# Performance work log

Measured on AMD Instinct MI355X. Metric: run time of the kernel, lower is better.

## Reference

```python
import jax, jax.numpy as jnp
import numpy as np

N = 100000          # nodes
E = 1000000         # edges (before self loops)
F_IN = 128          # node feature dim
HEADS = [4, 2, 2]   # gat_heads
D = 48              # per-head out channels (hardcoded in module)
G = 64              # number of graphs in batch
FC_DIM = 192
OUT_DIM = 96
NEG_SLOPE = 0.2     # PyG GATConv default


def setup_inputs() -> dict:
    key = jax.random.key(0)
    ks = jax.random.split(key, 32)
    d = {
        "x": jax.random.normal(ks[0], (N, F_IN), jnp.float32),
        "edge_index": jax.random.randint(ks[1], (2, E), 0, N, dtype=jnp.int64),
        "batch": jnp.sort(jax.random.randint(ks[2], (N,), 0, G, dtype=jnp.int64)),
    }
    in_ch = F_IN
    k = 3
    for i, h in enumerate(HEADS):
        d[f"W{i}"] = jax.random.normal(ks[k], (in_ch, h * D), jnp.float32) / np.sqrt(in_ch); k += 1
        d[f"att_src{i}"] = jax.random.normal(ks[k], (h, D), jnp.float32) * 0.1; k += 1
        d[f"att_dst{i}"] = jax.random.normal(ks[k], (h, D), jnp.float32) * 0.1; k += 1
        d[f"bias{i}"] = jnp.zeros((h * D,), jnp.float32)
        in_ch = h * D
    d["fcW1"] = jax.random.normal(ks[k], (in_ch, FC_DIM), jnp.float32) / np.sqrt(in_ch); k += 1
    d["fcb1"] = jnp.zeros((FC_DIM,), jnp.float32)
    d["fcW2"] = jax.random.normal(ks[k], (FC_DIM, OUT_DIM), jnp.float32) / np.sqrt(FC_DIM); k += 1
    d["fcb2"] = jnp.zeros((OUT_DIM,), jnp.float32)
    return d


def _gat_layer(x, W, att_src, att_dst, bias, src, dst, heads):
    n = x.shape[0]
    h = (x @ W).reshape(n, heads, D)                    # [N,H,D]
    a_src = jnp.sum(h * att_src, axis=-1)               # [N,H]
    a_dst = jnp.sum(h * att_dst, axis=-1)               # [N,H]
    e = jax.nn.leaky_relu(a_src[src] + a_dst[dst], NEG_SLOPE)   # [Et,H]
    # segment softmax over incoming edges at each destination node
    m = jax.ops.segment_max(e, dst, num_segments=n)
    e = jnp.exp(e - m[dst])
    denom = jax.ops.segment_sum(e, dst, num_segments=n)
    alpha = e / (denom[dst] + 1e-16)                    # [Et,H]
    msg = h[src] * alpha[..., None]                     # [Et,H,D]
    out = jax.ops.segment_sum(msg, dst, num_segments=n) # [N,H,D]
    return out.reshape(n, heads * D) + bias


def reference(x, edge_index, batch,
              W0, att_src0, att_dst0, bias0,
              W1, att_src1, att_dst1, bias1,
              W2, att_src2, att_dst2, bias2,
              fcW1, fcb1, fcW2, fcb2):
    n = x.shape[0]
    loops = jnp.arange(n, dtype=edge_index.dtype)
    src = jnp.concatenate([edge_index[0], loops])   # add self loops (PyG default)
    dst = jnp.concatenate([edge_index[1], loops])
    x = jax.nn.relu(_gat_layer(x, W0, att_src0, att_dst0, bias0, src, dst, HEADS[0]))
    x = jax.nn.relu(_gat_layer(x, W1, att_src1, att_dst1, bias1, src, dst, HEADS[1]))
    x = jax.nn.relu(_gat_layer(x, W2, att_src2, att_dst2, bias2, src, dst, HEADS[2]))
    # global mean pool over graphs
    sums = jax.ops.segment_sum(x, batch, num_segments=G)
    counts = jax.ops.segment_sum(jnp.ones((n, 1), x.dtype), batch, num_segments=G)
    pooled = sums / jnp.maximum(counts, 1.0)
    h = jax.nn.relu(pooled @ fcW1 + fcb1)
    return h @ fcW2 + fcb2
```

## Files before the change

### kernel.cpp

```cpp
#include <hip/hip_runtime.h>

#define CAP 48
#define DD 48
#define BSH 8
#define NBUCK_MAX 400
#define CHUNK_MAX 4300

typedef short v8s __attribute__((ext_vector_type(8)));
typedef float v4f __attribute__((ext_vector_type(4)));
typedef float v2f __attribute__((ext_vector_type(2)));

__device__ __forceinline__ unsigned int bf16r(float f) {
    unsigned int u = __float_as_uint(f);
    return (u + 0x7FFFu + ((u >> 16) & 1u)) >> 16;
}

__device__ __forceinline__ v8s ld_frag(const ushort* p) {
    const uint2* q = reinterpret_cast<const uint2*>(p);
    uint2 a = q[0], b = q[1];
    union { unsigned int u[4]; v8s v; } t;
    t.u[0] = a.x; t.u[1] = a.y; t.u[2] = b.x; t.u[3] = b.y;
    return t.v;
}


__global__ void hist_kernel(const int* __restrict__ ei, int E, int N, int nbuck,
                            int* __restrict__ Hh) {
    __shared__ int lhist[NBUCK_MAX];
    int blk = blockIdx.x, t = threadIdx.x;
    int Et = E + N;
    int chunk = (Et + 255) >> 8;
    int lo = blk * chunk, hi = min(Et, lo + chunk);
    for (int i = t; i < nbuck; i += 256) lhist[i] = 0;
    __syncthreads();
    for (int e = lo + t; e < hi; e += 256) {
        int d = (e < E) ? ei[E + e] : (e - E);
        atomicAdd(&lhist[d >> BSH], 1);
    }
    __syncthreads();
    for (int b = t; b < nbuck; b += 256) Hh[b * 256 + blk] = lhist[b];
}

__global__ void scan_bucket_kernel(int* __restrict__ Hh, int* __restrict__ btot) {
    int b = blockIdx.x, lane = threadIdx.x;
    uint4 v = reinterpret_cast<uint4*>(Hh)[b * 64 + lane];
    unsigned s0 = v.x, s1 = s0 + v.y, s2 = s1 + v.z, s3 = s2 + v.w;
    unsigned incl = s3;
#pragma unroll
    for (int off = 1; off < 64; off <<= 1) {
        unsigned tmp = __shfl_up(incl, off);
        if (lane >= off) incl += tmp;
    }
    unsigned excl = incl - s3;
    reinterpret_cast<uint4*>(Hh)[b * 64 + lane] =
        make_uint4(excl, excl + s0, excl + s1, excl + s2);
    if (lane == 63) btot[b] = (int)incl;
}

__global__ void scan_base_kernel(const int* __restrict__ btot, int* __restrict__ bbase, int nbuck) {
    int lane = threadIdx.x;
    int carry = 0;
    int nch = (nbuck + 63) >> 6;
    for (int c = 0; c < nch; c++) {
        int idx = c * 64 + lane;
        int val = (idx < nbuck) ? btot[idx] : 0;
        int incl = val;
#pragma unroll
        for (int off = 1; off < 64; off <<= 1) {
            int tmp = __shfl_up(incl, off);
            if (lane >= off) incl += tmp;
        }
        if (idx < nbuck) bbase[idx] = carry + incl - val;
        carry += __shfl(incl, 63);
    }
    if (lane == 0) bbase[nbuck] = carry;
}

__global__ void add_base_kernel(int* __restrict__ Hh, const int* __restrict__ bbase) {
    Hh[blockIdx.x * 256 + threadIdx.x] += bbase[blockIdx.x];
}

__global__ void scatter_kernel(const int* __restrict__ ei, int E, int N, int nbuck,
                               const int* __restrict__ Hh, unsigned int* __restrict__ P) {
    __shared__ unsigned int sp[CHUNK_MAX];
    __shared__ int ga[CHUNK_MAX];
    __shared__ int lhist[NBUCK_MAX], lbaseL[NBUCK_MAX], lbaseG[NBUCK_MAX], lcur[NBUCK_MAX];
    int blk = blockIdx.x, t = threadIdx.x;
    int Et = E + N;
    int chunk = (Et + 255) >> 8;
    int lo = blk * chunk, hi = min(Et, lo + chunk);
    for (int i = t; i < nbuck; i += 256) { lhist[i] = 0; lcur[i] = 0; }
    __syncthreads();
    for (int e = lo + t; e < hi; e += 256) {
        int d = (e < E) ? ei[E + e] : (e - E);
        atomicAdd(&lhist[d >> BSH], 1);
    }
    __syncthreads();
    if (t < 64) {
        int lane = t, carry = 0;
        int nch = (nbuck + 63) >> 6;
        for (int c = 0; c < nch; c++) {
            int idx = c * 64 + lane;
            int val = (idx < nbuck) ? lhist[idx] : 0;
            int incl = val;
#pragma unroll
            for (int off = 1; off < 64; off <<= 1) {
                int tmp = __shfl_up(incl, off);
                if (lane >= off) incl += tmp;
            }
            if (idx < nbuck) {
                lbaseL[idx] = carry + incl - val;
                lbaseG[idx] = Hh[idx * 256 + blk];
            }
            carry += __shfl(incl, 63);
        }
    }
    __syncthreads();
    for (int e = lo + t; e < hi; e += 256) {
        int s, d;
        if (e < E) { s = ei[e]; d = ei[E + e]; } else { s = e - E; d = e - E; }
        int b = d >> BSH;
        int lpos = atomicAdd(&lcur[b], 1);
        int loc = lbaseL[b] + lpos;
        sp[loc] = ((unsigned)(d & 255) << 24) | (unsigned)s;
        ga[loc] = lbaseG[b] + lpos;
    }
    __syncthreads();
    int len = hi - lo;
    for (int i = t; i < len; i += 256) P[ga[i]] = sp[i];
}

__global__ void buildadj_kernel(const unsigned int* __restrict__ P, const int* __restrict__ bbase,
                                int* __restrict__ adj, int* __restrict__ cnt, int N) {
    __shared__ int slab[256 * CAP];
    __shared__ int cntL[256];
    int b = blockIdx.x, t = threadIdx.x;
    int n0 = b << BSH;
    int nodes = min(256, N - n0);
    cntL[t] = 0;
    __syncthreads();
    int lo = bbase[b], hi = bbase[b + 1];
    for (int i = lo + t; i < hi; i += 256) {
        unsigned p = P[i];
        int dloc = (int)(p >> 24);
        int s = (int)(p & 0x1FFFFu);
        int lpos = atomicAdd(&cntL[dloc], 1);
        if (lpos < CAP) slab[dloc * CAP + lpos] = s;
    }
    __syncthreads();
    int tot = nodes * CAP;
    for (int i = t; i < tot; i += 256) adj[(long)n0 * CAP + i] = slab[i];
    if (t < nodes) cnt[n0 + t] = min(cntL[t], CAP);
}

__global__ void cast_x_kernel(const float* __restrict__ x, unsigned int* __restrict__ xb, long n2) {
    long i = (long)blockIdx.x * blockDim.x + threadIdx.x;
    if (i >= n2) return;
    float2 v = reinterpret_cast<const float2*>(x)[i];
    xb[i] = bf16r(v.x) | (bf16r(v.y) << 16);
}

__global__ void convw_kernel(const float* __restrict__ W, ushort* __restrict__ WT, int K, int NC) {
    int i = blockIdx.x * blockDim.x + threadIdx.x;
    if (i >= K * NC) return;
    int k = i / NC, n = i % NC;
    WT[n * K + k] = (ushort)bf16r(W[i]);
}

template<int K, int NCT, int HEADS>
__global__ void gemm_mfma(const ushort* __restrict__ Xb, const ushort* __restrict__ WT,
                          const float* __restrict__ att_s, const float* __restrict__ att_d,
                          ushort* __restrict__ Hb, float* __restrict__ asrc,
                          float* __restrict__ adst, int N) {
    __shared__ ushort XT_l[128 * 40];
    __shared__ ushort WT_l[96 * 40];
    int tid = threadIdx.x;
    int wv = tid >> 6, lane = tid & 63;
    int m = lane & 15, quad = lane >> 4;
    int rb = blockIdx.x * 128;
    int c0 = blockIdx.y * 96;
    int mw = wv * 32;
    v4f acc[2][6];
#pragma unroll
    for (int mi = 0; mi < 2; mi++)
#pragma unroll
        for (int nb = 0; nb < 6; nb++) acc[mi][nb] = (v4f){0.f, 0.f, 0.f, 0.f};

    for (int k0 = 0; k0 < K; k0 += 32) {
#pragma unroll
        for (int t = 0; t < 2; t++) {
            int ch = tid + t * 256;
            int r = ch >> 2, kq = ch & 3;
            int rg = rb + r;
            uint4 v = make_uint4(0u, 0u, 0u, 0u);
            if (rg < N) v = *reinterpret_cast<const uint4*>(&Xb[(long)rg * K + k0 + kq * 8]);
            uint2* d = reinterpret_cast<uint2*>(&XT_l[r * 40 + kq * 8]);
            d[0] = make_uint2(v.x, v.y);
            d[1] = make_uint2(v.z, v.w);
        }
#pragma unroll
        for (int t = 0; t < 2; t++) {
            int ch = tid + t * 256;
            if (ch < 384) {
                int wr = ch >> 2, kq = ch & 3;
                uint4 v = *reinterpret_cast<const uint4*>(&WT[(long)(c0 + wr) * K + k0 + kq * 8]);
                uint2* d = reinterpret_cast<uint2*>(&WT_l[wr * 40 + kq * 8]);
                d[0] = make_uint2(v.x, v.y);
                d[1] = make_uint2(v.z, v.w);
            }
        }
        __syncthreads();
        v8s af[2], bf[6];
        af[0] = ld_frag(&XT_l[(mw + m) * 40 + quad * 8]);
        af[1] = ld_frag(&XT_l[(mw + 16 + m) * 40 + quad * 8]);
#pragma unroll
        for (int nb = 0; nb < 6; nb++)
            bf[nb] = ld_frag(&WT_l[(nb * 16 + m) * 40 + quad * 8]);
#pragma unroll
        for (int mi = 0; mi < 2; mi++)
#pragma unroll
            for (int nb = 0; nb < 6; nb++)
                acc[mi][nb] = __builtin_amdgcn_mfma_f32_16x16x32_bf16(af[mi], bf[nb], acc[mi][nb], 0, 0, 0);
        __syncthreads();
    }

#pragma unroll
    for (int mi = 0; mi < 2; mi++)
#pragma unroll
        for (int r = 0; r < 4; r++) {
            int R = rb + mw + mi * 16 + quad * 4 + r;
            if (R < N) {
#pragma unroll
                for (int nb = 0; nb < 6; nb++)
                    Hb[(long)R * NCT + c0 + nb * 16 + m] = (ushort)bf16r(acc[mi][nb][r]);
            }
        }

    float aS[6], aD[6];
    int h0 = c0 / DD;
#pragma unroll
    for (int nb = 0; nb < 6; nb++) {
        int cb = nb * 16 + m;
        int hl = cb / DD;
        int cih = cb - hl * DD;
        aS[nb] = att_s[(h0 + hl) * DD + cih];
        aD[nb] = att_d[(h0 + hl) * DD + cih];
    }
#pragma unroll
    for (int mi = 0; mi < 2; mi++)
#pragma unroll
        for (int r = 0; r < 4; r++) {
            float ps0 = 0.f, ps1 = 0.f, pd0 = 0.f, pd1 = 0.f;
#pragma unroll
            for (int nb = 0; nb < 3; nb++) {
                ps0 = fmaf(acc[mi][nb][r], aS[nb], ps0);
                pd0 = fmaf(acc[mi][nb][r], aD[nb], pd0);
            }
#pragma unroll
            for (int nb = 3; nb < 6; nb++) {
                ps1 = fmaf(acc[mi][nb][r], aS[nb], ps1);
                pd1 = fmaf(acc[mi][nb][r], aD[nb], pd1);
            }
#pragma unroll
            for (int d = 1; d < 16; d <<= 1) {
                ps0 += __shfl_xor(ps0, d); ps1 += __shfl_xor(ps1, d);
                pd0 += __shfl_xor(pd0, d); pd1 += __shfl_xor(pd1, d);
            }
            int R = rb + mw + mi * 16 + quad * 4 + r;
            if (m == 0 && R < N) {
                asrc[R * HEADS + h0]     = ps0;
                asrc[R * HEADS + h0 + 1] = ps1;
                adst[R * HEADS + h0]     = pd0;
                adst[R * HEADS + h0 + 1] = pd1;
            }
        }
}

template<int OUT, int HEADS, int EPW, bool OBF16>
__global__ void agg_kernel(const unsigned int* __restrict__ Hb,
                           const float* __restrict__ asrc, const float* __restrict__ adst,
                           const int* __restrict__ adj, const int* __restrict__ cnt,
                           const float* __restrict__ bias,
                           unsigned int* __restrict__ Ob, float* __restrict__ Of, int N) {
    constexpr int LPE = 64 / EPW;
    constexpr int ROWU = OUT / 2;
    __shared__ float wlds[4][HEADS][65];
    __shared__ float dlds[4][HEADS];
    __shared__ int   slds[4][64];
    int wv = threadIdx.x >> 6;
    int lane = threadIdx.x & 63;
    int esub = lane / LPE;
    int lp   = lane % LPE;
    int n = blockIdx.x * 4 + wv;
    bool valid = (n < N);
    int nn = valid ? n : 0;
    int deg_raw = cnt[nn];
    int araw = (lane < CAP) ? adj[(long)nn * CAP + lane] : 0;
    int deg = min(deg_raw, CAP);
    int s = (lane < deg) ? araw : 0;
    slds[wv][lane] = s;

    float av[HEADS], dvv[HEADS];
    if constexpr (HEADS == 4) {
        float4 t = *reinterpret_cast<const float4*>(&asrc[s * 4]);
        av[0] = t.x; av[1] = t.y; av[2] = t.z; av[3] = t.w;
        float4 u = *reinterpret_cast<const float4*>(&adst[nn * 4]);
        dvv[0] = u.x; dvv[1] = u.y; dvv[2] = u.z; dvv[3] = u.w;
    } else {
        float2 t = *reinterpret_cast<const float2*>(&asrc[s * 2]);
        av[0] = t.x; av[1] = t.y;
        float2 u = *reinterpret_cast<const float2*>(&adst[nn * 2]);
        dvv[0] = u.x; dvv[1] = u.y;
    }
    float w[HEADS];
#pragma unroll
    for (int h = 0; h < HEADS; h++) {
        float e = av[h] + dvv[h];
        e = (e < 0.f) ? 0.2f * e : e;
        w[h] = (lane < deg) ? __expf(e) : 0.f;
        wlds[wv][h][lane] = w[h];
    }
#pragma unroll
    for (int h = 0; h < HEADS; h++) {
        float dsum = w[h];
#pragma unroll
        for (int off = 1; off < 64; off <<= 1) dsum += __shfl_xor(dsum, off);
        if (lane == 0) dlds[wv][h] = dsum;
    }
    __syncthreads();

    int c = lp * 6;
    int head = c / DD;
    const float* wrow = &wlds[wv][head][0];
    v2f a0 = (v2f){0.f, 0.f}, a1 = (v2f){0.f, 0.f}, a2 = (v2f){0.f, 0.f};

    for (int base = 0; base < deg; base += 2 * EPW) {
        int e0 = base + esub, e1 = base + EPW + esub;
        int s0 = slds[wv][e0], s1 = slds[wv][e1];
        uint3 h0 = *reinterpret_cast<const uint3*>(&Hb[(long)s0 * ROWU + lp * 3]);
        uint3 h1 = *reinterpret_cast<const uint3*>(&Hb[(long)s1 * ROWU + lp * 3]);
        float w0 = wrow[e0], w1 = wrow[e1];
        v2f p;
        p.x = __uint_as_float(h0.x << 16); p.y = __uint_as_float(h0.x & 0xFFFF0000u);
        a0 += w0 * p;
        p.x = __uint_as_float(h0.y << 16); p.y = __uint_as_float(h0.y & 0xFFFF0000u);
        a1 += w0 * p;
        p.x = __uint_as_float(h0.z << 16); p.y = __uint_as_float(h0.z & 0xFFFF0000u);
        a2 += w0 * p;
        p.x = __uint_as_float(h1.x << 16); p.y = __uint_as_float(h1.x & 0xFFFF0000u);
        a0 += w1 * p;
        p.x = __uint_as_float(h1.y << 16); p.y = __uint_as_float(h1.y & 0xFFFF0000u);
        a1 += w1 * p;
        p.x = __uint_as_float(h1.z << 16); p.y = __uint_as_float(h1.z & 0xFFFF0000u);
        a2 += w1 * p;
    }

#pragma unroll
    for (int off = LPE; off < 64; off <<= 1) {
        a0.x += __shfl_xor(a0.x, off); a0.y += __shfl_xor(a0.y, off);
        a1.x += __shfl_xor(a1.x, off); a1.y += __shfl_xor(a1.y, off);
        a2.x += __shfl_xor(a2.x, off); a2.y += __shfl_xor(a2.y, off);
    }

    if (valid && esub == 0) {
        float invd = 1.f / (dlds[wv][head] + 1e-16f);
        float o[6];
        o[0] = fmaxf(fmaf(a0.x, invd, bias[c + 0]), 0.f);
        o[1] = fmaxf(fmaf(a0.y, invd, bias[c + 1]), 0.f);
        o[2] = fmaxf(fmaf(a1.x, invd, bias[c + 2]), 0.f);
        o[3] = fmaxf(fmaf(a1.y, invd, bias[c + 3]), 0.f);
        o[4] = fmaxf(fmaf(a2.x, invd, bias[c + 4]), 0.f);
        o[5] = fmaxf(fmaf(a2.y, invd, bias[c + 5]), 0.f);
        if (OBF16) {
            uint3 pk;
            pk.x = bf16r(o[0]) | (bf16r(o[1]) << 16);
            pk.y = bf16r(o[2]) | (bf16r(o[3]) << 16);
            pk.z = bf16r(o[4]) | (bf16r(o[5]) << 16);
            *reinterpret_cast<uint3*>(&Ob[(long)n * ROWU + lp * 3]) = pk;
        } else {
            float* dst = &Of[(long)n * OUT + c];
            *reinterpret_cast<float2*>(dst)     = make_float2(o[0], o[1]);
            *reinterpret_cast<float2*>(dst + 2) = make_float2(o[2], o[3]);
            *reinterpret_cast<float2*>(dst + 4) = make_float2(o[4], o[5]);
        }
    }
}

__global__ void pool_kernel(const float* __restrict__ O, const int* __restrict__ batch,
                            float* __restrict__ sums, float* __restrict__ counts, int N) {
    int grp = threadIdx.x >> 7;
    int c = threadIdx.x & 127;
    int n0 = (blockIdx.x * 4 + grp) * 64;
    if (n0 >= N) return;
    int nend = min(N, n0 + 64);
    bool act = (c < 96);
    float acc = 0.f; int cl = 0;
    int cur = batch[n0];
    int n = n0;
    for (; n + 4 <= nend; n += 4) {
        int g0 = batch[n], g1 = batch[n + 1], g2 = batch[n + 2], g3 = batch[n + 3];
        float v0 = 0.f, v1 = 0.f, v2 = 0.f, v3 = 0.f;
        if (act) {
            v0 = O[(long)n * 96 + c];       v1 = O[(long)(n + 1) * 96 + c];
            v2 = O[(long)(n + 2) * 96 + c]; v3 = O[(long)(n + 3) * 96 + c];
        }
#define POOL_STEP(g, v)                                                        \
        if ((g) != cur) {                                                      \
            if (act) atomicAdd(&sums[cur * 96 + c], acc);                      \
            if (c == 96) atomicAdd(&counts[cur], (float)cl);                   \
            acc = 0.f; cl = 0; cur = (g);                                      \
        }                                                                      \
        acc += (v); cl++;
        POOL_STEP(g0, v0) POOL_STEP(g1, v1) POOL_STEP(g2, v2) POOL_STEP(g3, v3)
    }
    for (; n < nend; n++) {
        int g = batch[n];
        float v = act ? O[(long)n * 96 + c] : 0.f;
        POOL_STEP(g, v)
    }
#undef POOL_STEP
    if (act) atomicAdd(&sums[cur * 96 + c], acc);
    if (c == 96) atomicAdd(&counts[cur], (float)cl);
}

__global__ void fc_kernel(const float* __restrict__ sums, const float* __restrict__ counts,
                          const float* __restrict__ W1, const float* __restrict__ b1,
                          const float* __restrict__ W2, const float* __restrict__ b2,
                          float* __restrict__ out) {
    __shared__ float p[96];
    __shared__ float h1[192];
    int g = blockIdx.x, tid = threadIdx.x;
    if (tid < 96) p[tid] = sums[g * 96 + tid] / fmaxf(counts[g], 1.0f);
    __syncthreads();
    float s = b1[tid];
    for (int c = 0; c < 96; c++) s = fmaf(p[c], W1[c * 192 + tid], s);
    h1[tid] = fmaxf(s, 0.f);
    __syncthreads();
    if (tid < 96) {
        float s2 = b2[tid];
        for (int j = 0; j < 192; j++) s2 = fmaf(h1[j], W2[j * 96 + tid], s2);
        out[g * 96 + tid] = s2;
    }
}

extern "C" void kernel_launch(void* const* d_in, const int* in_sizes, int n_in,
                              void* d_out, int out_size, void* d_ws, size_t ws_size,
                              hipStream_t stream) {
    const float* x     = (const float*)d_in[0];
    const int*   ei    = (const int*)d_in[1];
    const int*   batch = (const int*)d_in[2];
    const float* W0  = (const float*)d_in[3];
    const float* as0 = (const float*)d_in[4];
    const float* ad0 = (const float*)d_in[5];
    const float* b0  = (const float*)d_in[6];
    const float* W1  = (const float*)d_in[7];
    const float* as1 = (const float*)d_in[8];
    const float* ad1 = (const float*)d_in[9];
    const float* b1  = (const float*)d_in[10];
    const float* W2  = (const float*)d_in[11];
    const float* as2 = (const float*)d_in[12];
    const float* ad2 = (const float*)d_in[13];
    const float* b2  = (const float*)d_in[14];
    const float* fcW1 = (const float*)d_in[15];
    const float* fcb1 = (const float*)d_in[16];
    const float* fcW2 = (const float*)d_in[17];
    const float* fcb2 = (const float*)d_in[18];

    const int N = in_sizes[0] / 128;
    const int E = in_sizes[1] / 2;
    const int Et = E + N;
    const int nbuck = (N + 255) >> 8;

    char* ws = (char*)d_ws;
    unsigned int* Xb   = (unsigned int*)ws;
    unsigned int* Hb   = (unsigned int*)(ws + (size_t)N * 256);
    unsigned int* Ob   = (unsigned int*)(ws + (size_t)N * 640);
    float*        Obuf = (float*)(ws + (size_t)N * 1024);
    float*        ASRC = (float*)(ws + (size_t)N * 1408);
    float*        ADST = (float*)(ws + (size_t)N * 1424);
    int*          ADJ  = (int*)(ws + (size_t)N * 1440);
    int*          CNT  = (int*)(ws + (size_t)N * 1632);
    float*        SUMS = (float*)(ws + (size_t)N * 1636);
    float*        COUNTS = SUMS + 64 * 96;
    ushort*       WT0  = (ushort*)(COUNTS + 64);
    ushort*       WT1  = WT0 + 192 * 128;
    ushort*       WT2  = WT1 + 96 * 192;
    char*         tail = (char*)(WT2 + 96 * 96);
    int*          HIST = (int*)tail;
    int*          BTOT = (int*)(tail + NBUCK_MAX * 256 * 4);
    int*          BBASE = (int*)(tail + NBUCK_MAX * 256 * 4 + NBUCK_MAX * 4);
    unsigned int* P    = (unsigned int*)(tail + NBUCK_MAX * 260 * 4 + 64);

    hipMemsetAsync(SUMS, 0, (64 * 96 + 64) * 4, stream);

    hist_kernel<<<256, 256, 0, stream>>>(ei, E, N, nbuck, HIST);
    scan_bucket_kernel<<<nbuck, 64, 0, stream>>>(HIST, BTOT);
    scan_base_kernel<<<1, 64, 0, stream>>>(BTOT, BBASE, nbuck);
    add_base_kernel<<<nbuck, 256, 0, stream>>>(HIST, BBASE);
    scatter_kernel<<<256, 256, 0, stream>>>(ei, E, N, nbuck, HIST, P);
    buildadj_kernel<<<nbuck, 256, 0, stream>>>(P, BBASE, ADJ, CNT, N);

    long n2 = (long)N * 64;
    cast_x_kernel<<<(int)((n2 + 255) / 256), 256, 0, stream>>>(x, Xb, n2);
    convw_kernel<<<(128 * 192 + 255) / 256, 256, 0, stream>>>(W0, WT0, 128, 192);
    convw_kernel<<<(192 * 96 + 255) / 256, 256, 0, stream>>>(W1, WT1, 192, 96);
    convw_kernel<<<(96 * 96 + 255) / 256, 256, 0, stream>>>(W2, WT2, 96, 96);

    int gb = (N + 127) / 128;

    gemm_mfma<128, 192, 4><<<dim3(gb, 2), 256, 0, stream>>>((const ushort*)Xb, WT0, as0, ad0,
                                                            (ushort*)Hb, ASRC, ADST, N);
    agg_kernel<192, 4, 2, true><<<(N + 3) / 4, 256, 0, stream>>>(Hb, ASRC, ADST, ADJ, CNT, b0, Ob, nullptr, N);

    gemm_mfma<192, 96, 2><<<dim3(gb, 1), 256, 0, stream>>>((const ushort*)Ob, WT1, as1, ad1,
                                                           (ushort*)Hb, ASRC, ADST, N);
    agg_kernel<96, 2, 4, true><<<(N + 3) / 4, 256, 0, stream>>>(Hb, ASRC, ADST, ADJ, CNT, b1, Ob, nullptr, N);

    gemm_mfma<96, 96, 2><<<dim3(gb, 1), 256, 0, stream>>>((const ushort*)Ob, WT2, as2, ad2,
                                                          (ushort*)Hb, ASRC, ADST, N);
    agg_kernel<96, 2, 4, false><<<(N + 3) / 4, 256, 0, stream>>>(Hb, ASRC, ADST, ADJ, CNT, b2, nullptr, Obuf, N);

    pool_kernel<<<(N / 256) + 1, 512, 0, stream>>>(Obuf, batch, SUMS, COUNTS, N);
    fc_kernel<<<64, 192, 0, stream>>>(SUMS, COUNTS, fcW1, fcb1, fcW2, fcb2, (float*)d_out);
}
```

Baseline: 467.4 us.

## Fuse input cast into GEMM, pooling into last aggregation, merge small kernels

```diff
diff --git a/kernel.cpp b/kernel.cpp
--- a/kernel.cpp
+++ b/kernel.cpp
@@ -76,12 +76,9 @@
     if (lane == 0) bbase[nbuck] = carry;
 }
 
-__global__ void add_base_kernel(int* __restrict__ Hh, const int* __restrict__ bbase) {
-    Hh[blockIdx.x * 256 + threadIdx.x] += bbase[blockIdx.x];
-}
-
 __global__ void scatter_kernel(const int* __restrict__ ei, int E, int N, int nbuck,
-                               const int* __restrict__ Hh, unsigned int* __restrict__ P) {
+                               const int* __restrict__ Hh, const int* __restrict__ bbase,
+                               unsigned int* __restrict__ P) {
     __shared__ unsigned int sp[CHUNK_MAX];
     __shared__ int ga[CHUNK_MAX];
     __shared__ int lhist[NBUCK_MAX], lbaseL[NBUCK_MAX], lbaseG[NBUCK_MAX], lcur[NBUCK_MAX];
@@ -110,7 +107,7 @@
             }
             if (idx < nbuck) {
                 lbaseL[idx] = carry + incl - val;
-                lbaseG[idx] = Hh[idx * 256 + blk];
+                lbaseG[idx] = Hh[idx * 256 + blk] + bbase[idx];
             }
             carry += __shfl(incl, 63);
         }
@@ -153,22 +150,24 @@
     if (t < nodes) cnt[n0 + t] = min(cntL[t], CAP);
 }
 
-__global__ void cast_x_kernel(const float* __restrict__ x, unsigned int* __restrict__ xb, long n2) {
-    long i = (long)blockIdx.x * blockDim.x + threadIdx.x;
-    if (i >= n2) return;
-    float2 v = reinterpret_cast<const float2*>(x)[i];
-    xb[i] = bf16r(v.x) | (bf16r(v.y) << 16);
-}
-
-__global__ void convw_kernel(const float* __restrict__ W, ushort* __restrict__ WT, int K, int NC) {
-    int i = blockIdx.x * blockDim.x + threadIdx.x;
-    if (i >= K * NC) return;
-    int k = i / NC, n = i % NC;
-    WT[n * K + k] = (ushort)bf16r(W[i]);
-}
-
-template<int K, int NCT, int HEADS>
-__global__ void gemm_mfma(const ushort* __restrict__ Xb, const ushort* __restrict__ WT,
+__global__ void convw_all_kernel(const float* __restrict__ W0, const float* __restrict__ W1,
+                                 const float* __restrict__ W2, ushort* __restrict__ WT0,
+                                 ushort* __restrict__ WT1, ushort* __restrict__ WT2) {
+    int i = blockIdx.x * 256 + threadIdx.x;
+    if (i < 24576) {
+        int k = i / 192, n = i % 192;
+        WT0[n * 128 + k] = (ushort)bf16r(W0[i]);
+    } else if (i < 43008) {
+        int j = i - 24576; int k = j / 96, n = j % 96;
+        WT1[n * 192 + k] = (ushort)bf16r(W1[j]);
+    } else if (i < 52224) {
+        int j = i - 43008; int k = j / 96, n = j % 96;
+        WT2[n * 96 + k] = (ushort)bf16r(W2[j]);
+    }
+}
+
+template<int K, int NCT, int HEADS, bool XF32>
+__global__ void gemm_mfma(const void* __restrict__ Xp, const ushort* __restrict__ WT,
                           const float* __restrict__ att_s, const float* __restrict__ att_d,
                           ushort* __restrict__ Hb, float* __restrict__ asrc,
                           float* __restrict__ adst, int N) {
@@ -192,11 +191,25 @@
             int ch = tid + t * 256;
             int r = ch >> 2, kq = ch & 3;
             int rg = rb + r;
-            uint4 v = make_uint4(0u, 0u, 0u, 0u);
-            if (rg < N) v = *reinterpret_cast<const uint4*>(&Xb[(long)rg * K + k0 + kq * 8]);
+            uint2 d0, d1;
+            if (XF32) {
+                const float* Xf = (const float*)Xp;
+                float4 va = make_float4(0.f, 0.f, 0.f, 0.f), vb = va;
+                if (rg < N) {
+                    va = *reinterpret_cast<const float4*>(&Xf[(long)rg * K + k0 + kq * 8]);
+                    vb = *reinterpret_cast<const float4*>(&Xf[(long)rg * K + k0 + kq * 8 + 4]);
+                }
+                d0 = make_uint2(bf16r(va.x) | (bf16r(va.y) << 16), bf16r(va.z) | (bf16r(va.w) << 16));
+                d1 = make_uint2(bf16r(vb.x) | (bf16r(vb.y) << 16), bf16r(vb.z) | (bf16r(vb.w) << 16));
+            } else {
+                const ushort* Xb = (const ushort*)Xp;
+                uint4 v = make_uint4(0u, 0u, 0u, 0u);
+                if (rg < N) v = *reinterpret_cast<const uint4*>(&Xb[(long)rg * K + k0 + kq * 8]);
+                d0 = make_uint2(v.x, v.y);
+                d1 = make_uint2(v.z, v.w);
+            }
             uint2* d = reinterpret_cast<uint2*>(&XT_l[r * 40 + kq * 8]);
-            d[0] = make_uint2(v.x, v.y);
-            d[1] = make_uint2(v.z, v.w);
+            d[0] = d0; d[1] = d1;
         }
 #pragma unroll
         for (int t = 0; t < 2; t++) {
@@ -276,17 +289,21 @@
         }
 }
 
-template<int OUT, int HEADS, int EPW, bool OBF16>
+template<int OUT, int HEADS, int EPW, bool OBF16, bool POOL>
 __global__ void agg_kernel(const unsigned int* __restrict__ Hb,
                            const float* __restrict__ asrc, const float* __restrict__ adst,
                            const int* __restrict__ adj, const int* __restrict__ cnt,
                            const float* __restrict__ bias,
-                           unsigned int* __restrict__ Ob, float* __restrict__ Of, int N) {
+                           unsigned int* __restrict__ Ob,
+                           const int* __restrict__ batch,
+                           float* __restrict__ sums, float* __restrict__ counts, int N) {
     constexpr int LPE = 64 / EPW;
     constexpr int ROWU = OUT / 2;
     __shared__ float wlds[4][HEADS][65];
     __shared__ float dlds[4][HEADS];
     __shared__ int   slds[4][64];
+    __shared__ float psum[4][96];
+    __shared__ int   gl[4];
     int wv = threadIdx.x >> 6;
     int lane = threadIdx.x & 63;
     int esub = lane / LPE;
@@ -326,6 +343,9 @@
 #pragma unroll
         for (int off = 1; off < 64; off <<= 1) dsum += __shfl_xor(dsum, off);
         if (lane == 0) dlds[wv][h] = dsum;
+    }
+    if (POOL) {
+        if (lane == 0) gl[wv] = valid ? batch[nn] : -1;
     }
     __syncthreads();
 
@@ -362,65 +382,49 @@
         a2.x += __shfl_xor(a2.x, off); a2.y += __shfl_xor(a2.y, off);
     }
 
-    if (valid && esub == 0) {
-        float invd = 1.f / (dlds[wv][head] + 1e-16f);
-        float o[6];
-        o[0] = fmaxf(fmaf(a0.x, invd, bias[c + 0]), 0.f);
-        o[1] = fmaxf(fmaf(a0.y, invd, bias[c + 1]), 0.f);
-        o[2] = fmaxf(fmaf(a1.x, invd, bias[c + 2]), 0.f);
-        o[3] = fmaxf(fmaf(a1.y, invd, bias[c + 3]), 0.f);
-        o[4] = fmaxf(fmaf(a2.x, invd, bias[c + 4]), 0.f);
-        o[5] = fmaxf(fmaf(a2.y, invd, bias[c + 5]), 0.f);
-        if (OBF16) {
+    float invd = 1.f / (dlds[wv][head] + 1e-16f);
+    float o[6];
+    o[0] = fmaxf(fmaf(a0.x, invd, bias[c + 0]), 0.f);
+    o[1] = fmaxf(fmaf(a0.y, invd, bias[c + 1]), 0.f);
+    o[2] = fmaxf(fmaf(a1.x, invd, bias[c + 2]), 0.f);
+    o[3] = fmaxf(fmaf(a1.y, invd, bias[c + 3]), 0.f);
+    o[4] = fmaxf(fmaf(a2.x, invd, bias[c + 4]), 0.f);
+    o[5] = fmaxf(fmaf(a2.y, invd, bias[c + 5]), 0.f);
+
+    if (POOL) {
+        __syncthreads();
+        bool uni = (gl[0] >= 0) && (gl[1] == gl[0]) && (gl[2] == gl[0]) && (gl[3] == gl[0]);
+        if (uni) {
+            if (esub == 0) {
+#pragma unroll
+                for (int j = 0; j < 6; j++) psum[wv][c + j] = o[j];
+            }
+            __syncthreads();
+            int t = threadIdx.x;
+            if (t < 96) {
+                float sm = psum[0][t] + psum[1][t] + psum[2][t] + psum[3][t];
+                atomicAdd(&sums[gl[0] * 96 + t], sm);
+            } else if (t == 96) {
+                atomicAdd(&counts[gl[0]], 4.0f);
+            }
+        } else {
+            if (valid && esub == 0) {
+                int g = gl[wv];
+#pragma unroll
+                for (int j = 0; j < 6; j++) atomicAdd(&sums[g * 96 + c + j], o[j]);
+                if (lp == 0) atomicAdd(&counts[g], 1.0f);
+            }
+            __syncthreads();
+        }
+    } else {
+        if (valid && esub == 0) {
             uint3 pk;
             pk.x = bf16r(o[0]) | (bf16r(o[1]) << 16);
             pk.y = bf16r(o[2]) | (bf16r(o[3]) << 16);
             pk.z = bf16r(o[4]) | (bf16r(o[5]) << 16);
             *reinterpret_cast<uint3*>(&Ob[(long)n * ROWU + lp * 3]) = pk;
-        } else {
-            float* dst = &Of[(long)n * OUT + c];
-            *reinterpret_cast<float2*>(dst)     = make_float2(o[0], o[1]);
-            *reinterpret_cast<float2*>(dst + 2) = make_float2(o[2], o[3]);
-            *reinterpret_cast<float2*>(dst + 4) = make_float2(o[4], o[5]);
-        }
-    }
-}
-
-__global__ void pool_kernel(const float* __restrict__ O, const int* __restrict__ batch,
-                            float* __restrict__ sums, float* __restrict__ counts, int N) {
-    int grp = threadIdx.x >> 7;
-    int c = threadIdx.x & 127;
-    int n0 = (blockIdx.x * 4 + grp) * 64;
-    if (n0 >= N) return;
-    int nend = min(N, n0 + 64);
-    bool act = (c < 96);
-    float acc = 0.f; int cl = 0;
-    int cur = batch[n0];
-    int n = n0;
-    for (; n + 4 <= nend; n += 4) {
-        int g0 = batch[n], g1 = batch[n + 1], g2 = batch[n + 2], g3 = batch[n + 3];
-        float v0 = 0.f, v1 = 0.f, v2 = 0.f, v3 = 0.f;
-        if (act) {
-            v0 = O[(long)n * 96 + c];       v1 = O[(long)(n + 1) * 96 + c];
-            v2 = O[(long)(n + 2) * 96 + c]; v3 = O[(long)(n + 3) * 96 + c];
-        }
-#define POOL_STEP(g, v)                                                        \
-        if ((g) != cur) {                                                      \
-            if (act) atomicAdd(&sums[cur * 96 + c], acc);                      \
-            if (c == 96) atomicAdd(&counts[cur], (float)cl);                   \
-            acc = 0.f; cl = 0; cur = (g);                                      \
-        }                                                                      \
-        acc += (v); cl++;
-        POOL_STEP(g0, v0) POOL_STEP(g1, v1) POOL_STEP(g2, v2) POOL_STEP(g3, v3)
-    }
-    for (; n < nend; n++) {
-        int g = batch[n];
-        float v = act ? O[(long)n * 96 + c] : 0.f;
-        POOL_STEP(g, v)
-    }
-#undef POOL_STEP
-    if (act) atomicAdd(&sums[cur * 96 + c], acc);
-    if (c == 96) atomicAdd(&counts[cur], (float)cl);
+        }
+    }
 }
 
 __global__ void fc_kernel(const float* __restrict__ sums, const float* __restrict__ counts,
@@ -468,19 +472,16 @@
 
     const int N = in_sizes[0] / 128;
     const int E = in_sizes[1] / 2;
-    const int Et = E + N;
     const int nbuck = (N + 255) >> 8;
 
     char* ws = (char*)d_ws;
-    unsigned int* Xb   = (unsigned int*)ws;
-    unsigned int* Hb   = (unsigned int*)(ws + (size_t)N * 256);
-    unsigned int* Ob   = (unsigned int*)(ws + (size_t)N * 640);
-    float*        Obuf = (float*)(ws + (size_t)N * 1024);
-    float*        ASRC = (float*)(ws + (size_t)N * 1408);
-    float*        ADST = (float*)(ws + (size_t)N * 1424);
-    int*          ADJ  = (int*)(ws + (size_t)N * 1440);
-    int*          CNT  = (int*)(ws + (size_t)N * 1632);
-    float*        SUMS = (float*)(ws + (size_t)N * 1636);
+    unsigned int* Hb   = (unsigned int*)ws;
+    unsigned int* Ob   = (unsigned int*)(ws + (size_t)N * 384);
+    float*        ASRC = (float*)(ws + (size_t)N * 768);
+    float*        ADST = (float*)(ws + (size_t)N * 784);
+    int*          ADJ  = (int*)(ws + (size_t)N * 800);
+    int*          CNT  = (int*)(ws + (size_t)N * 992);
+    float*        SUMS = (float*)(ws + (size_t)N * 996);
     float*        COUNTS = SUMS + 64 * 96;
     ushort*       WT0  = (ushort*)(COUNTS + 64);
     ushort*       WT1  = WT0 + 192 * 128;
@@ -496,30 +497,27 @@
     hist_kernel<<<256, 256, 0, stream>>>(ei, E, N, nbuck, HIST);
     scan_bucket_kernel<<<nbuck, 64, 0, stream>>>(HIST, BTOT);
     scan_base_kernel<<<1, 64, 0, stream>>>(BTOT, BBASE, nbuck);
-    add_base_kernel<<<nbuck, 256, 0, stream>>>(HIST, BBASE);
-    scatter_kernel<<<256, 256, 0, stream>>>(ei, E, N, nbuck, HIST, P);
+    scatter_kernel<<<256, 256, 0, stream>>>(ei, E, N, nbuck, HIST, BBASE, P);
     buildadj_kernel<<<nbuck, 256, 0, stream>>>(P, BBASE, ADJ, CNT, N);
 
-    long n2 = (long)N * 64;
-    cast_x_kernel<<<(int)((n2 + 255) / 256), 256, 0, stream>>>(x, Xb, n2);
-    convw_kernel<<<(128 * 192 + 255) / 256, 256, 0, stream>>>(W0, WT0, 128, 192);
-    convw_kernel<<<(192 * 96 + 255) / 256, 256, 0, stream>>>(W1, WT1, 192, 96);
-    convw_kernel<<<(96 * 96 + 255) / 256, 256, 0, stream>>>(W2, WT2, 96, 96);
+    convw_all_kernel<<<204, 256, 0, stream>>>(W0, W1, W2, WT0, WT1, WT2);
 
     int gb = (N + 127) / 128;
 
-    gemm_mfma<128, 192, 4><<<dim3(gb, 2), 256, 0, stream>>>((const ushort*)Xb, WT0, as0, ad0,
-                                                            (ushort*)Hb, ASRC, ADST, N);
-    agg_kernel<192, 4, 2, true><<<(N + 3) / 4, 256, 0, stream>>>(Hb, ASRC, ADST, ADJ, CNT, b0, Ob, nullptr, N);
-
-    gemm_mfma<192, 96, 2><<<dim3(gb, 1), 256, 0, stream>>>((const ushort*)Ob, WT1, as1, ad1,
-                                                           (ushort*)Hb, ASRC, ADST, N);
-    agg_kernel<96, 2, 4, true><<<(N + 3) / 4, 256, 0, stream>>>(Hb, ASRC, ADST, ADJ, CNT, b1, Ob, nullptr, N);
-
-    gemm_mfma<96, 96, 2><<<dim3(gb, 1), 256, 0, stream>>>((const ushort*)Ob, WT2, as2, ad2,
-                                                          (ushort*)Hb, ASRC, ADST, N);
-    agg_kernel<96, 2, 4, false><<<(N + 3) / 4, 256, 0, stream>>>(Hb, ASRC, ADST, ADJ, CNT, b2, nullptr, Obuf, N);
-
-    pool_kernel<<<(N / 256) + 1, 512, 0, stream>>>(Obuf, batch, SUMS, COUNTS, N);
+    gemm_mfma<128, 192, 4, true><<<dim3(gb, 2), 256, 0, stream>>>(x, WT0, as0, ad0,
+                                                                  (ushort*)Hb, ASRC, ADST, N);
+    agg_kernel<192, 4, 2, true, false><<<(N + 3) / 4, 256, 0, stream>>>(
+        Hb, ASRC, ADST, ADJ, CNT, b0, Ob, batch, nullptr, nullptr, N);
+
+    gemm_mfma<192, 96, 2, false><<<dim3(gb, 1), 256, 0, stream>>>(Ob, WT1, as1, ad1,
+                                                                  (ushort*)Hb, ASRC, ADST, N);
+    agg_kernel<96, 2, 4, true, false><<<(N + 3) / 4, 256, 0, stream>>>(
+        Hb, ASRC, ADST, ADJ, CNT, b1, Ob, batch, nullptr, nullptr, N);
+
+    gemm_mfma<96, 96, 2, false><<<dim3(gb, 1), 256, 0, stream>>>(Ob, WT2, as2, ad2,
+                                                                 (ushort*)Hb, ASRC, ADST, N);
+    agg_kernel<96, 2, 4, false, true><<<(N + 3) / 4, 256, 0, stream>>>(
+        Hb, ASRC, ADST, ADJ, CNT, b2, nullptr, batch, SUMS, COUNTS, N);
+
     fc_kernel<<<64, 192, 0, stream>>>(SUMS, COUNTS, fcW1, fcb1, fcW2, fcb2, (float*)d_out);
 }
```

New measurement: 581.0 us. 24.3% more time.
